# Optimization experiments

Measured on AMD Instinct MI355X. Metric: run time of the kernel, lower is better.

The kernel has to match this reference:

```python
import jax, jax.numpy as jnp
import numpy as np

D_MODEL = 1024
NUM_HEADS = 16
D_K = D_MODEL // NUM_HEADS


def setup_inputs() -> dict:
    key = jax.random.key(0)
    ks = jax.random.split(key, 9)
    s = 1.0 / np.sqrt(D_MODEL)
    X = jax.random.normal(ks[0], (4, 2048, D_MODEL), dtype=jnp.float32)
    Wq = jax.random.uniform(ks[1], (D_MODEL, D_MODEL), jnp.float32, -s, s)
    bq = jax.random.uniform(ks[2], (D_MODEL,), jnp.float32, -s, s)
    Wk = jax.random.uniform(ks[3], (D_MODEL, D_MODEL), jnp.float32, -s, s)
    bk = jax.random.uniform(ks[4], (D_MODEL,), jnp.float32, -s, s)
    Wv = jax.random.uniform(ks[5], (D_MODEL, D_MODEL), jnp.float32, -s, s)
    bv = jax.random.uniform(ks[6], (D_MODEL,), jnp.float32, -s, s)
    Wo = jax.random.uniform(ks[7], (D_MODEL, D_MODEL), jnp.float32, -s, s)
    bo = jax.random.uniform(ks[8], (D_MODEL,), jnp.float32, -s, s)
    return {"X": X, "Wq": Wq, "bq": bq, "Wk": Wk, "bk": bk,
            "Wv": Wv, "bv": bv, "Wo": Wo, "bo": bo}


def reference(X, Wq, bq, Wk, bk, Wv, bv, Wo, bo):
    B, n, d = X.shape
    # Linear layers: y = x @ W^T + b (torch Linear convention)
    Q = X @ Wq.T + bq
    K = X @ Wk.T + bk
    V = X @ Wv.T + bv
    # [B, n, H, d_k] -> [B, H, n, d_k]
    Q = Q.reshape(B, n, NUM_HEADS, D_K).transpose(0, 2, 1, 3)
    K = K.reshape(B, n, NUM_HEADS, D_K).transpose(0, 2, 1, 3)
    V = V.reshape(B, n, NUM_HEADS, D_K).transpose(0, 2, 1, 3)
    scores = jnp.einsum('bhqd,bhkd->bhqk', Q, K) / jnp.sqrt(jnp.float32(D_K))
    attn = jax.nn.softmax(scores, axis=-1)  # [B, H, n, n]
    out = jnp.einsum('bhqk,bhkd->bhqd', attn, V)
    out = out.transpose(0, 2, 1, 3).reshape(B, n, d)
    return out @ Wo.T + bo
```

## Files before the change

kernel.cpp:

```cpp
#include <hip/hip_runtime.h>
#include <hip/hip_bf16.h>
#include <stdint.h>

typedef __hip_bfloat16 bf16;
typedef __bf16 bf16x8 __attribute__((ext_vector_type(8)));
typedef float floatx4 __attribute__((ext_vector_type(4)));

#define MFMA16(a, b, c) __builtin_amdgcn_mfma_f32_16x16x32_bf16((a), (b), (c), 0, 0, 0)

typedef __attribute__((address_space(3))) uint32_t lds_u32;
typedef const __attribute__((address_space(1))) uint32_t gbl_u32;

__device__ __forceinline__ void async16(const void* g, void* s) {
    __builtin_amdgcn_global_load_lds((gbl_u32*)g, (lds_u32*)s, 16, 0, 0);
}

__device__ __forceinline__ unsigned short f2bf_rne(float f) {
    union { float f; unsigned u; } v; v.f = f;
    const unsigned u = v.u;
    return (unsigned short)((u + 0x7FFFu + ((u >> 16) & 1u)) >> 16);
}
__device__ __forceinline__ unsigned pk2(float a, float b) {
    __hip_bfloat162 h = __float22bfloat162_rn(make_float2(a, b));
    return *(unsigned*)&h;
}

#define A_X   0L
#define A_WQ  8388608L
#define A_WK  9437184L
#define A_WV  10485760L
#define A_WO  11534336L
#define A_END 12582912L

__global__ __launch_bounds__(256) void cvt5(
    const float* __restrict__ s0, const float* __restrict__ s1,
    const float* __restrict__ s2, const float* __restrict__ s3,
    const float* __restrict__ s4, unsigned short* __restrict__ dst)
{
    const long beg[6] = {A_X, A_WQ, A_WK, A_WV, A_WO, A_END};
    const float* srcs[5] = {s0, s1, s2, s3, s4};
    const long nchunk = A_END / 8;
    for (long c = (long)blockIdx.x * 256 + threadIdx.x; c < nchunk;
         c += (long)gridDim.x * 256) {
        const long off = c * 8;
        int s = 0;
#pragma unroll
        for (int i = 1; i < 5; ++i) if (off >= beg[i]) s = i;
        const float* sp = srcs[s] + (off - beg[s]);
        const uint4 lo = *(const uint4*)(sp);
        const uint4 hi = *(const uint4*)(sp + 4);
        const float* fl = (const float*)&lo;
        const float* fh = (const float*)&hi;
        uint4 o;
        o.x = pk2(fl[0], fl[1]); o.y = pk2(fl[2], fl[3]);
        o.z = pk2(fh[0], fh[1]); o.w = pk2(fh[2], fh[3]);
        *(uint4*)(dst + off) = o;
    }
}

template <int CFP32, int TRANSV>
__global__ __launch_bounds__(256, 2) void gemm_bt3(
    const bf16* __restrict__ A,
    const bf16* __restrict__ W0, const bf16* __restrict__ W1, const bf16* __restrict__ W2,
    const float* __restrict__ b0, const float* __restrict__ b1, const float* __restrict__ b2,
    void* __restrict__ C0, void* __restrict__ C1, void* __restrict__ C2)
{
    __shared__ bf16 As[128 * 64];
    __shared__ bf16 Bs[128 * 64];

    const int tid = threadIdx.x;
    const int which = blockIdx.y >> 3;
    const int nt = blockIdx.y & 7;
    const bf16* __restrict__ W   = (which == 0) ? W0 : ((which == 1) ? W1 : W2);
    const float* __restrict__ bb = (which == 0) ? b0 : ((which == 1) ? b1 : b2);
    void* __restrict__ C         = (which == 0) ? C0 : ((which == 1) ? C1 : C2);

    const int m0 = blockIdx.x * 128;
    const int n0 = nt * 128;

    const int w  = tid >> 6;
    const int l  = tid & 63;
    const int lr = l & 15;
    const int q  = l >> 4;
    const int wm = (w & 1) * 64;
    const int wn = (w >> 1) * 64;
    const int wbase = tid & 0xC0;

    floatx4 acc[4][4];
#pragma unroll
    for (int i = 0; i < 4; ++i)
#pragma unroll
        for (int j = 0; j < 4; ++j)
            acc[i][j] = (floatx4){0.f, 0.f, 0.f, 0.f};

#pragma unroll 1
    for (int kt = 0; kt < 16; ++kt) {
        __syncthreads();
#pragma unroll
        for (int r = 0; r < 4; ++r) {
            const int u   = r * 256 + tid;
            const int row = u >> 3;
            const int kg  = u & 7;
            const int kgg = kg ^ (row & 7);
            const size_t goffA = (size_t)(m0 + row) * 1024 + kt * 64 + kgg * 8;
            const size_t goffB = (size_t)(n0 + row) * 1024 + kt * 64 + kgg * 8;
            bf16* dA = As + (size_t)(r * 256 + wbase) * 8;
            bf16* dB = Bs + (size_t)(r * 256 + wbase) * 8;
            async16(A + goffA, dA);
            async16(W + goffB, dB);
        }
        asm volatile("s_waitcnt vmcnt(0)" ::: "memory");
        __syncthreads();

#pragma unroll
        for (int ks = 0; ks < 2; ++ks) {
            bf16x8 av[4], bv[4];
#pragma unroll
            for (int i = 0; i < 4; ++i) {
                const int row = wm + i * 16 + lr;
                const int kg  = (ks * 4 + q) ^ (row & 7);
                av[i] = *(const bf16x8*)(As + row * 64 + kg * 8);
            }
#pragma unroll
            for (int j = 0; j < 4; ++j) {
                const int row = wn + j * 16 + lr;
                const int kg  = (ks * 4 + q) ^ (row & 7);
                bv[j] = *(const bf16x8*)(Bs + row * 64 + kg * 8);
            }
#pragma unroll
            for (int i = 0; i < 4; ++i)
#pragma unroll
                for (int j = 0; j < 4; ++j)
                    acc[i][j] = MFMA16(av[i], bv[j], acc[i][j]);
        }
    }

    if (TRANSV && which == 2) {
#pragma unroll
        for (int j = 0; j < 4; ++j) {
            const int col = n0 + wn + j * 16 + lr;
            const float bj = bb[col];
            const int h = col >> 6, d = col & 63;
#pragma unroll
            for (int i = 0; i < 4; ++i) {
                const int row0 = m0 + wm + i * 16 + q * 4;
                const int b = row0 >> 11;
                const int key = row0 & 2047;
                uint2 ov;
                ov.x = pk2(acc[i][j][0] + bj, acc[i][j][1] + bj);
                ov.y = pk2(acc[i][j][2] + bj, acc[i][j][3] + bj);
                *(uint2*)((unsigned short*)C +
                          ((size_t)(b * 16 + h) * 64 + d) * 2048 + key) = ov;
            }
        }
    } else {
#pragma unroll
        for (int j = 0; j < 4; ++j) {
            const int col = n0 + wn + j * 16 + lr;
            const float bj = bb[col];
#pragma unroll
            for (int i = 0; i < 4; ++i) {
#pragma unroll
                for (int r = 0; r < 4; ++r) {
                    const int row = m0 + wm + i * 16 + q * 4 + r;
                    const float val = acc[i][j][r] + bj;
                    if (CFP32)
                        ((float*)C)[(long)row * 1024 + col] = val;
                    else
                        ((unsigned short*)C)[(long)row * 1024 + col] = f2bf_rne(val);
                }
            }
        }
    }
}

__global__ __launch_bounds__(256, 2) void attn_flash(
    const bf16* __restrict__ Q, const bf16* __restrict__ K, const bf16* __restrict__ VT,
    bf16* __restrict__ AO)
{
    __shared__ bf16 Ks[64 * 64];
    __shared__ bf16 Vt[64 * 64];
    __shared__ bf16 Ps[128 * 64];

    const int tid = threadIdx.x;
    const int b = blockIdx.y >> 4, h = blockIdx.y & 15;
    const int q0 = blockIdx.x * 128;
    const size_t base = ((size_t)b * 2048) * 1024 + (size_t)h * 64;
    const size_t vtb  = (size_t)(b * 16 + h) * 64 * 2048;

    const int w  = tid >> 6;
    const int l  = tid & 63;
    const int lr = l & 15;
    const int q  = l >> 4;

    const int krow = tid >> 3, kkg = tid & 7;
    const int vd = tid >> 2,   vko = tid & 3;

    bf16x8 qb[2][2];
#pragma unroll
    for (int i = 0; i < 2; ++i)
#pragma unroll
        for (int ks = 0; ks < 2; ++ks)
            qb[i][ks] = *(const bf16x8*)(Q + base +
                (size_t)(q0 + w * 32 + i * 16 + lr) * 1024 + ks * 32 + q * 8);

    uint4 kreg0 = *(const uint4*)(K + base + (size_t)krow * 1024 + kkg * 8);
    uint4 kreg1 = *(const uint4*)(K + base + (size_t)(32 + krow) * 1024 + kkg * 8);
    uint4 vreg0 = *(const uint4*)(VT + vtb + (size_t)vd * 2048 + vko * 8);
    uint4 vreg1 = *(const uint4*)(VT + vtb + (size_t)vd * 2048 + 32 + vko * 8);

    floatx4 O[2][4];
#pragma unroll
    for (int i = 0; i < 2; ++i)
#pragma unroll
        for (int d = 0; d < 4; ++d) O[i][d] = (floatx4){0.f, 0.f, 0.f, 0.f};
    float mprev[2] = {-1e30f, -1e30f}, lsum[2] = {0.f, 0.f};
    const float cs = 0.18033688011112042f;

#pragma unroll 1
    for (int kt = 0; kt < 32; ++kt) {
        if (kt) __syncthreads();

        *(uint4*)(Ks + krow * 64 + ((kkg ^ (krow & 7)) * 8))        = kreg0;
        *(uint4*)(Ks + (32 + krow) * 64 + ((kkg ^ (krow & 7)) * 8)) = kreg1;
        *(uint4*)(Vt + vd * 64 + ((vko ^ (vd & 7)) * 8))            = vreg0;
        *(uint4*)(Vt + vd * 64 + (((4 + vko) ^ (vd & 7)) * 8))      = vreg1;
        __syncthreads();

        if (kt < 31) {
            const size_t kb = base + (size_t)((kt + 1) * 64) * 1024;
            kreg0 = *(const uint4*)(K + kb + (size_t)krow * 1024 + kkg * 8);
            kreg1 = *(const uint4*)(K + kb + (size_t)(32 + krow) * 1024 + kkg * 8);
            const size_t vb2 = vtb + (size_t)vd * 2048 + (kt + 1) * 64;
            vreg0 = *(const uint4*)(VT + vb2 + vko * 8);
            vreg1 = *(const uint4*)(VT + vb2 + 32 + vko * 8);
        }

        floatx4 s[2][4];
#pragma unroll
        for (int i = 0; i < 2; ++i)
#pragma unroll
            for (int t = 0; t < 4; ++t)
                s[i][t] = (floatx4){0.f, 0.f, 0.f, 0.f};
#pragma unroll
        for (int ks = 0; ks < 2; ++ks) {
            bf16x8 kb[4];
#pragma unroll
            for (int t = 0; t < 4; ++t) {
                const int R = t * 16 + lr;
                kb[t] = *(const bf16x8*)(Ks + R * 64 + (((ks * 4 + q) ^ (R & 7)) * 8));
            }
            __builtin_amdgcn_s_setprio(1);
#pragma unroll
            for (int i = 0; i < 2; ++i)
#pragma unroll
                for (int t = 0; t < 4; ++t)
                    s[i][t] = MFMA16(kb[t], qb[i][ks], s[i][t]);
            __builtin_amdgcn_s_setprio(0);
        }

#pragma unroll
        for (int i = 0; i < 2; ++i) {
            float t0 = fmaxf(fmaxf(s[i][0][0], s[i][0][1]), s[i][0][2]);
            float t1 = fmaxf(fmaxf(s[i][0][3], s[i][1][0]), s[i][1][1]);
            float t2 = fmaxf(fmaxf(s[i][1][2], s[i][1][3]), s[i][2][0]);
            float t3 = fmaxf(fmaxf(s[i][2][1], s[i][2][2]), s[i][2][3]);
            float t4 = fmaxf(fmaxf(s[i][3][0], s[i][3][1]), s[i][3][2]);
            const float vm = fmaxf(fmaxf(fmaxf(t0, t1), fmaxf(t2, t3)),
                                   fmaxf(t4, s[i][3][3]));
            const float mt = vm * cs;
            if (__any(mt > mprev[i] + 8.f)) {
                float vr = fmaxf(mt, __shfl_xor(mt, 16));
                vr = fmaxf(vr, __shfl_xor(vr, 32));
                const float mnew  = fmaxf(mprev[i], vr);
                const float alpha = exp2f(mprev[i] - mnew);
                mprev[i] = mnew;
                lsum[i] *= alpha;
#pragma unroll
                for (int d = 0; d < 4; ++d) O[i][d] *= alpha;
            }
            const float mcur = mprev[i];
            float rsum = 0.f;
#pragma unroll
            for (int t = 0; t < 4; ++t)
#pragma unroll
                for (int r = 0; r < 4; ++r) {
                    const float p = exp2f(s[i][t][r] * cs - mcur);
                    s[i][t][r] = p;
                    rsum += p;
                }
            lsum[i] += rsum;

            const int R = w * 32 + i * 16 + lr;
#pragma unroll
            for (int t = 0; t < 4; ++t) {
                uint2 ph;
                ph.x = pk2(s[i][t][0], s[i][t][1]);
                ph.y = pk2(s[i][t][2], s[i][t][3]);
                *(uint2*)((unsigned short*)Ps + R * 64 +
                          (((2 * t + (q >> 1)) ^ (R & 7)) * 8) + (q & 1) * 4) = ph;
            }
        }
        asm volatile("s_waitcnt lgkmcnt(0)" ::: "memory");

#pragma unroll
        for (int kc = 0; kc < 2; ++kc) {
            bf16x8 va[4], pb[2];
#pragma unroll
            for (int dt = 0; dt < 4; ++dt) {
                const int R = dt * 16 + lr;
                va[dt] = *(const bf16x8*)(Vt + R * 64 + (((kc * 4 + q) ^ (R & 7)) * 8));
            }
#pragma unroll
            for (int i = 0; i < 2; ++i) {
                const int R = w * 32 + i * 16 + lr;
                pb[i] = *(const bf16x8*)(Ps + R * 64 + (((kc * 4 + q) ^ (R & 7)) * 8));
            }
            __builtin_amdgcn_s_setprio(1);
#pragma unroll
            for (int i = 0; i < 2; ++i)
#pragma unroll
                for (int dt = 0; dt < 4; ++dt)
                    O[i][dt] = MFMA16(va[dt], pb[i], O[i][dt]);
            __builtin_amdgcn_s_setprio(0);
        }
    }

#pragma unroll
    for (int i = 0; i < 2; ++i) {
        float ls = lsum[i];
        ls += __shfl_xor(ls, 16);
        ls += __shfl_xor(ls, 32);
        const float inv = 1.f / ls;
        const int row = q0 + w * 32 + i * 16 + lr;
#pragma unroll
        for (int dt = 0; dt < 4; ++dt) {
            uint2 oh;
            oh.x = pk2(O[i][dt][0] * inv, O[i][dt][1] * inv);
            oh.y = pk2(O[i][dt][2] * inv, O[i][dt][3] * inv);
            *(uint2*)((unsigned short*)AO + base + (size_t)row * 1024 +
                      dt * 16 + q * 4) = oh;
        }
    }
}

extern "C" void kernel_launch(void* const* d_in, const int* in_sizes, int n_in,
                              void* d_out, int out_size, void* d_ws, size_t ws_size,
                              hipStream_t stream) {
    (void)in_sizes; (void)n_in; (void)out_size; (void)ws_size;
    const float* X  = (const float*)d_in[0];
    const float* Wq = (const float*)d_in[1];
    const float* bq = (const float*)d_in[2];
    const float* Wk = (const float*)d_in[3];
    const float* bk = (const float*)d_in[4];
    const float* Wv = (const float*)d_in[5];
    const float* bv = (const float*)d_in[6];
    const float* Wo = (const float*)d_in[7];
    const float* bo = (const float*)d_in[8];
    float* out = (float*)d_out;

    unsigned short* arena = (unsigned short*)d_ws;
    bf16* Xb  = (bf16*)(arena + A_X);
    bf16* Wqb = (bf16*)(arena + A_WQ);
    bf16* Wkb = (bf16*)(arena + A_WK);
    bf16* Wvb = (bf16*)(arena + A_WV);
    bf16* Wob = (bf16*)(arena + A_WO);

    const size_t SZ = (size_t)8192 * 1024;
    bf16* Qb  = (bf16*)(arena + A_END);
    bf16* Kb  = Qb + SZ;
    bf16* VTb = Kb + SZ;
    bf16* AOb = VTb + SZ;

    cvt5<<<dim3(1536), dim3(256), 0, stream>>>(X, Wq, Wk, Wv, Wo, arena);

    gemm_bt3<0, 1><<<dim3(64, 24), dim3(256), 0, stream>>>(
        Xb, Wqb, Wkb, Wvb, bq, bk, bv, (void*)Qb, (void*)Kb, (void*)VTb);

    attn_flash<<<dim3(16, 64), dim3(256), 0, stream>>>(Qb, Kb, VTb, AOb);

    gemm_bt3<1, 0><<<dim3(64, 8), dim3(256), 0, stream>>>(
        AOb, Wob, Wob, Wob, bo, bo, bo, (void*)out, (void*)out, (void*)out);
}
```

Baseline: 306.5 us.

## Keep P in registers via permuted K rows and double-buffer K/V LDS tiles

K rows are loaded in a permuted order, so each lane's score accumulators line up with the operand layout the PV MFMA expects. The probabilities can then be packed straight from registers instead of going through an LDS round trip (Ps buffer, stores, waitcnt, reloads). K and V tiles are also double-buffered in LDS, which removes the barrier at the top of each iteration. The K swizzle gains an extra XOR term to match the new row pattern. LDS use stays about the same because Ps is dropped.

```diff
diff --git a/kernel.cpp b/kernel.cpp
--- a/kernel.cpp
+++ b/kernel.cpp
@@ -174,13 +174,16 @@
     }
 }
 
+__device__ __forceinline__ int swzk(int R) {
+    return (R & 7) ^ (((R >> 3) & 1) << 2);
+}
+
 __global__ __launch_bounds__(256, 2) void attn_flash(
     const bf16* __restrict__ Q, const bf16* __restrict__ K, const bf16* __restrict__ VT,
     bf16* __restrict__ AO)
 {
-    __shared__ bf16 Ks[64 * 64];
-    __shared__ bf16 Vt[64 * 64];
-    __shared__ bf16 Ps[128 * 64];
+    __shared__ bf16 Ks[2][64 * 64];
+    __shared__ bf16 Vt[2][64 * 64];
 
     const int tid = threadIdx.x;
     const int b = blockIdx.y >> 4, h = blockIdx.y & 15;
@@ -195,6 +198,7 @@
 
     const int krow = tid >> 3, kkg = tid & 7;
     const int vd = tid >> 2,   vko = tid & 3;
+    const int ksw = kkg ^ swzk(krow);
 
     bf16x8 qb[2][2];
 #pragma unroll
@@ -219,18 +223,19 @@
 
 #pragma unroll 1
     for (int kt = 0; kt < 32; ++kt) {
-        if (kt) __syncthreads();
-
-        *(uint4*)(Ks + krow * 64 + ((kkg ^ (krow & 7)) * 8))        = kreg0;
-        *(uint4*)(Ks + (32 + krow) * 64 + ((kkg ^ (krow & 7)) * 8)) = kreg1;
-        *(uint4*)(Vt + vd * 64 + ((vko ^ (vd & 7)) * 8))            = vreg0;
-        *(uint4*)(Vt + vd * 64 + (((4 + vko) ^ (vd & 7)) * 8))      = vreg1;
+        bf16* __restrict__ Kc = Ks[kt & 1];
+        bf16* __restrict__ Vc = Vt[kt & 1];
+
+        *(uint4*)(Kc + krow * 64 + ksw * 8)                          = kreg0;
+        *(uint4*)(Kc + (32 + krow) * 64 + ksw * 8)                   = kreg1;
+        *(uint4*)(Vc + vd * 64 + ((vko ^ (vd & 7)) * 8))             = vreg0;
+        *(uint4*)(Vc + vd * 64 + (((4 + vko) ^ (vd & 7)) * 8))       = vreg1;
         __syncthreads();
 
         if (kt < 31) {
-            const size_t kb = base + (size_t)((kt + 1) * 64) * 1024;
-            kreg0 = *(const uint4*)(K + kb + (size_t)krow * 1024 + kkg * 8);
-            kreg1 = *(const uint4*)(K + kb + (size_t)(32 + krow) * 1024 + kkg * 8);
+            const size_t kb_ = base + (size_t)((kt + 1) * 64) * 1024;
+            kreg0 = *(const uint4*)(K + kb_ + (size_t)krow * 1024 + kkg * 8);
+            kreg1 = *(const uint4*)(K + kb_ + (size_t)(32 + krow) * 1024 + kkg * 8);
             const size_t vb2 = vtb + (size_t)vd * 2048 + (kt + 1) * 64;
             vreg0 = *(const uint4*)(VT + vb2 + vko * 8);
             vreg1 = *(const uint4*)(VT + vb2 + 32 + vko * 8);
@@ -247,8 +252,9 @@
             bf16x8 kb[4];
 #pragma unroll
             for (int t = 0; t < 4; ++t) {
-                const int R = t * 16 + lr;
-                kb[t] = *(const bf16x8*)(Ks + R * 64 + (((ks * 4 + q) ^ (R & 7)) * 8));
+                const int R = (t & 1) * 32 + (t >> 1) * 4 + (lr >> 2) * 8 + (lr & 3);
+                kb[t] = *(const bf16x8*)(Kc + R * 64 +
+                                         (((ks * 4 + q) ^ swzk(R)) * 8));
             }
             __builtin_amdgcn_s_setprio(1);
 #pragma unroll
@@ -290,31 +296,26 @@
                     rsum += p;
                 }
             lsum[i] += rsum;
-
-            const int R = w * 32 + i * 16 + lr;
-#pragma unroll
-            for (int t = 0; t < 4; ++t) {
-                uint2 ph;
-                ph.x = pk2(s[i][t][0], s[i][t][1]);
-                ph.y = pk2(s[i][t][2], s[i][t][3]);
-                *(uint2*)((unsigned short*)Ps + R * 64 +
-                          (((2 * t + (q >> 1)) ^ (R & 7)) * 8) + (q & 1) * 4) = ph;
-            }
-        }
-        asm volatile("s_waitcnt lgkmcnt(0)" ::: "memory");
+        }
 
 #pragma unroll
         for (int kc = 0; kc < 2; ++kc) {
-            bf16x8 va[4], pb[2];
+            bf16x8 va[4];
 #pragma unroll
             for (int dt = 0; dt < 4; ++dt) {
                 const int R = dt * 16 + lr;
-                va[dt] = *(const bf16x8*)(Vt + R * 64 + (((kc * 4 + q) ^ (R & 7)) * 8));
-            }
+                va[dt] = *(const bf16x8*)(Vc + R * 64 +
+                                          (((kc * 4 + q) ^ (R & 7)) * 8));
+            }
+            bf16x8 pb[2];
 #pragma unroll
             for (int i = 0; i < 2; ++i) {
-                const int R = w * 32 + i * 16 + lr;
-                pb[i] = *(const bf16x8*)(Ps + R * 64 + (((kc * 4 + q) ^ (R & 7)) * 8));
+                union { uint4 u; bf16x8 v; } pw;
+                pw.u.x = pk2(s[i][kc][0], s[i][kc][1]);
+                pw.u.y = pk2(s[i][kc][2], s[i][kc][3]);
+                pw.u.z = pk2(s[i][kc + 2][0], s[i][kc + 2][1]);
+                pw.u.w = pk2(s[i][kc + 2][2], s[i][kc + 2][3]);
+                pb[i] = pw.v;
             }
             __builtin_amdgcn_s_setprio(1);
 #pragma unroll
```

After: 294.2 us. 1.04x faster.
